# Optimization experiments

Measured on AMD Instinct MI355X. Metric: run time of the kernel, lower is better.

## Reference

```python
import jax, jax.numpy as jnp
import numpy as np

B, T, OBS = 16, 4095, 128
HID, NH, FF, NL = 256, 8, 1024, 4
DH = HID // NH
ACT = 32
KEPS = 0.001   # performer kernel_epsilon (generalized attention default)
LNEPS = 1e-6   # flax LayerNorm default eps


def setup_inputs() -> dict:
    key = jax.random.key(0)
    ks = list(jax.random.split(key, 16))
    s = 0.02
    r = lambda k, shape: jax.random.normal(k, shape, jnp.float32) * s
    return {
        "hidden_state": jnp.zeros((B, 1, HID), jnp.float32),
        "ins": jax.random.normal(ks[0], (B, T, OBS), jnp.float32),
        "resets": jax.random.randint(ks[1], (B,), 0, 2).astype(bool),
        "emb_W": r(ks[2], (OBS, HID)), "emb_b": jnp.zeros((HID,), jnp.float32),
        "Wq": r(ks[3], (NL, HID, NH, DH)), "bq": jnp.zeros((NL, NH, DH), jnp.float32),
        "Wk": r(ks[4], (NL, HID, NH, DH)), "bk": jnp.zeros((NL, NH, DH), jnp.float32),
        "Wv": r(ks[5], (NL, HID, NH, DH)), "bv": jnp.zeros((NL, NH, DH), jnp.float32),
        "Wo": r(ks[6], (NL, NH, DH, HID)), "bo": jnp.zeros((NL, HID), jnp.float32),
        "ln1_s": jnp.ones((NL, HID), jnp.float32), "ln1_b": jnp.zeros((NL, HID), jnp.float32),
        "W1": r(ks[7], (NL, HID, FF)), "b1": jnp.zeros((NL, FF), jnp.float32),
        "W2": r(ks[8], (NL, FF, HID)), "b2": jnp.zeros((NL, HID), jnp.float32),
        "ln2_s": jnp.ones((NL, HID), jnp.float32), "ln2_b": jnp.zeros((NL, HID), jnp.float32),
        "qp_W": r(ks[9], (HID, ACT)), "qp_b": jnp.zeros((ACT,), jnp.float32),
    }


def layer_norm(x, scale, bias):
    m = x.mean(-1, keepdims=True)
    v = ((x - m) ** 2).mean(-1, keepdims=True)
    return (x - m) * jax.lax.rsqrt(v + LNEPS) * scale + bias


def favor_attention(q, k, v):
    # FAVOR+ generalized attention with deterministic relu features (no random
    # projection, make_fast_generalized_attention defaults), bidirectional,
    # renormalized. q,k,v: [B, L, H, Dh]; feature dim M == Dh.
    qp = jax.nn.relu(q) + KEPS
    kp = jax.nn.relu(k) + KEPS
    kv = jnp.einsum('blhm,blhd->bhmd', kp, v)            # [B,H,M,Dh]
    num = jnp.einsum('blhm,bhmd->blhd', qp, kv)           # [B,L,H,Dh]
    den = jnp.einsum('blhm,bhm->blh', qp, kp.sum(axis=1))  # [B,L,H]
    return num / den[..., None]


def encoder_block(x, Wq, bq, Wk, bk, Wv, bv, Wo, bo, ln1_s, ln1_b, W1, b1, W2, b2, ln2_s, ln2_b):
    q = jnp.einsum('bld,dhm->blhm', x, Wq) + bq
    k = jnp.einsum('bld,dhm->blhm', x, Wk) + bk
    v = jnp.einsum('bld,dhm->blhm', x, Wv) + bv
    a = favor_attention(q, k, v)
    o = jnp.einsum('blhm,hmd->bld', a, Wo) + bo
    x = o + o  # faithful to source: x = attn(x); x = x + dropout(x)
    x = layer_norm(x, ln1_s, ln1_b)
    h = jax.nn.relu(x @ W1 + b1) @ W2 + b2
    h = h + h  # same residual quirk on the FFN branch
    return layer_norm(h, ln2_s, ln2_b)


def reference(hidden_state, ins, resets, emb_W, emb_b, Wq, bq, Wk, bk, Wv, bv, Wo, bo, ln1_s, ln1_b, W1, b1, W2, b2, ln2_s, ln2_b, qp_W, qp_b):
    emb = ins @ emb_W + emb_b                         # [B, T, HID]
    hs = jnp.where(resets[:, None, None], 0.0, hidden_state)
    x = jnp.concatenate([hs, emb], axis=-2)           # [B, 1+T, HID]
    for i in range(NL):
        x = encoder_block(x, Wq[i], bq[i], Wk[i], bk[i], Wv[i], bv[i], Wo[i], bo[i],
                          ln1_s[i], ln1_b[i], W1[i], b1[i], W2[i], b2[i], ln2_s[i], ln2_b[i])
    new_hidden = x[..., 0:1, :]                       # carry token
    q_vals = new_hidden @ qp_W + qp_b                 # [B, 1, ACT]
    return new_hidden, q_vals
```

## Files before the change

kernel.cpp:

```cpp
#include <hip/hip_runtime.h>


typedef unsigned short bf16_t;
typedef __attribute__((ext_vector_type(8))) short short8;
typedef __attribute__((ext_vector_type(4))) float float4v;

#define NB 16
#define LSEQ 4096
#define MROWS (NB * LSEQ)
#define HIDD 256
#define NHEAD 8
#define DHEAD 32
#define FFD 1024
#define NLAY 4
#define KEPS_F 1e-3f
#define LNEPS_F 1e-6f
#define KV_ELEMS (NB * NHEAD * 32 * 33)

__device__ __forceinline__ float b2f(bf16_t h) {
    return __uint_as_float(((unsigned int)h) << 16);
}
__device__ __forceinline__ bf16_t f2b(float f) {
    unsigned int u = __float_as_uint(f);
    u += 0x7fffu + ((u >> 16) & 1u);
    return (bf16_t)(u >> 16);
}

#define GLOAD_LDS16(g, l)                                                     \
    __builtin_amdgcn_global_load_lds(                                         \
        (const __attribute__((address_space(1))) void*)(g),                   \
        (__attribute__((address_space(3))) void*)(l), 16, 0, 0)

__global__ __launch_bounds__(256) void conv_transpose_kernel(
    const float* __restrict__ in, bf16_t* __restrict__ out, int R, int C,
    size_t ils, size_t ols)
{
    __shared__ float tile[32][33];
    const size_t ib = (size_t)blockIdx.z * ils;
    const size_t ob = (size_t)blockIdx.z * ols;
    const int r0 = blockIdx.y * 32, c0 = blockIdx.x * 32;
    const int tx = threadIdx.x & 31, ty = threadIdx.x >> 5;
#pragma unroll
    for (int rr = ty; rr < 32; rr += 8)
        tile[rr][tx] = in[ib + (size_t)(r0 + rr) * C + c0 + tx];
    __syncthreads();
#pragma unroll
    for (int rr = ty; rr < 32; rr += 8)
        out[ob + (size_t)(c0 + rr) * R + r0 + tx] = f2b(tile[tx][rr]);
}

__global__ __launch_bounds__(256) void concat_bias_kernel(
    const float* __restrict__ bq, const float* __restrict__ bk,
    const float* __restrict__ bv, float* __restrict__ bqkv)
{
    const int l = blockIdx.x, j = threadIdx.x;
    bqkv[l * 768 + j]       = bq[l * 256 + j];
    bqkv[l * 768 + 256 + j] = bk[l * 256 + j];
    bqkv[l * 768 + 512 + j] = bv[l * 256 + j];
}

__global__ __launch_bounds__(256) void prep_a_kernel(
    const float* __restrict__ ins, bf16_t* __restrict__ Ain)
{
    const int row = blockIdx.x * 2 + (threadIdx.x >> 7);
    const int j = threadIdx.x & 127;
    const int b = row >> 12, l = row & (LSEQ - 1);
    bf16_t v = 0;
    if (l != 0) v = f2b(ins[((size_t)b * 4095 + (l - 1)) * 128 + j]);
    Ain[(size_t)row * 128 + j] = v;
}

__global__ __launch_bounds__(256) void fix_row0_kernel(
    const float* __restrict__ hidden, const int* __restrict__ resets,
    bf16_t* __restrict__ X)
{
    const int b = blockIdx.x, j = threadIdx.x;
    float v = resets[b] ? 0.f : hidden[b * HIDD + j];
    X[((size_t)b * LSEQ) * HIDD + j] = f2b(v);
}

template <int MODE>
__global__ __launch_bounds__(512) void gemm_mfma(
    const bf16_t* __restrict__ A, const bf16_t* __restrict__ WT,
    const float* __restrict__ bias, bf16_t* __restrict__ C,
    int M, int N, int K, int lda, int ldc)
{
    __shared__ __align__(16) bf16_t As[128 * 64];
    __shared__ __align__(16) bf16_t Bs[256 * 64];
    const int tid = threadIdx.x;
    const int wave = tid >> 6, lane = tid & 63;
    const int bm = blockIdx.y * 128, bn = blockIdx.x * 256;
    const int quad = lane >> 4, mr = lane & 15;
    const int mxor = mr & 7;
    const int wm0 = (wave & 1) * 64;
    const int wn0 = (wave >> 1) * 64;

    float4v acc[4][4];
#pragma unroll
    for (int i = 0; i < 4; i++)
#pragma unroll
        for (int j = 0; j < 4; j++) acc[i][j] = (float4v)(0.f);

    for (int k0 = 0; k0 < K; k0 += 64) {
#pragma unroll
        for (int it = 0; it < 2; it++) {
            const int c = it * 512 + tid;
            const int r = c >> 3;
            const int kofs = ((c & 7) ^ (r & 7)) * 8;
            GLOAD_LDS16(A + (size_t)(bm + r) * lda + k0 + kofs, &As[c * 8]);
        }
#pragma unroll
        for (int it = 0; it < 4; it++) {
            const int c = it * 512 + tid;
            const int r = c >> 3;
            const int kofs = ((c & 7) ^ (r & 7)) * 8;
            GLOAD_LDS16(WT + (size_t)(bn + r) * K + k0 + kofs, &Bs[c * 8]);
        }
        __syncthreads();
#pragma unroll
        for (int kk = 0; kk < 8; kk += 4) {
            short8 a[4], b[4];
#pragma unroll
            for (int i = 0; i < 4; i++)
                a[i] = *(const short8*)&As[((wm0 + i * 16 + mr) * 8 + ((quad + kk) ^ mxor)) * 8];
#pragma unroll
            for (int j = 0; j < 4; j++)
                b[j] = *(const short8*)&Bs[((wn0 + j * 16 + mr) * 8 + ((quad + kk) ^ mxor)) * 8];
#pragma unroll
            for (int i = 0; i < 4; i++)
#pragma unroll
                for (int j = 0; j < 4; j++)
                    acc[i][j] = __builtin_amdgcn_mfma_f32_16x16x32_bf16(
                        a[i], b[j], acc[i][j], 0, 0, 0);
        }
        __syncthreads();
    }

    float bcol[4];
#pragma unroll
    for (int j = 0; j < 4; j++) bcol[j] = bias[bn + wn0 + j * 16 + mr];
#pragma unroll
    for (int i = 0; i < 4; i++) {
#pragma unroll
        for (int r = 0; r < 4; r++) {
            const int grow = bm + wm0 + i * 16 + quad * 4 + r;
            bf16_t* crow = C + (size_t)grow * ldc + bn + wn0 + mr;
#pragma unroll
            for (int j = 0; j < 4; j++) {
                float v = acc[i][j][r] + bcol[j];
                if (MODE == 1) v = fmaxf(v, 0.f);
                crow[j * 16] = f2b(v);
            }
        }
    }
}

__global__ __launch_bounds__(512) void gemm_ln_mfma(
    const bf16_t* __restrict__ A, const bf16_t* __restrict__ WT,
    const float* __restrict__ bias, const float* __restrict__ sc,
    const float* __restrict__ bi, bf16_t* __restrict__ out,
    int K, int lda)
{
    __shared__ __align__(16) bf16_t As[128 * 64];
    __shared__ __align__(16) bf16_t Bs[256 * 64];
    __shared__ float red[8][64][2];
    __shared__ float fin[128][2];

    const int tid = threadIdx.x;
    const int wave = tid >> 6, lane = tid & 63;
    const int bm = blockIdx.x * 128;
    const int quad = lane >> 4, mr = lane & 15;
    const int mxor = mr & 7;
    const int wm0 = (wave & 1) * 64;
    const int wn0 = (wave >> 1) * 64;

    float4v acc[4][4];
#pragma unroll
    for (int i = 0; i < 4; i++)
#pragma unroll
        for (int j = 0; j < 4; j++) acc[i][j] = (float4v)(0.f);

    for (int k0 = 0; k0 < K; k0 += 64) {
#pragma unroll
        for (int it = 0; it < 6; it++) {
            const int c = it * 512 + tid;
            if (c < 1024) {
                const int r = c >> 3;
                const int kofs = ((c & 7) ^ (r & 7)) * 8;
                GLOAD_LDS16(A + (size_t)(bm + r) * lda + k0 + kofs, &As[c * 8]);
            } else {
                const int cb = c - 1024;
                const int r = cb >> 3;
                const int kofs = ((cb & 7) ^ (r & 7)) * 8;
                GLOAD_LDS16(WT + (size_t)r * K + k0 + kofs, &Bs[cb * 8]);
            }
        }
        __syncthreads();
#pragma unroll
        for (int kk = 0; kk < 8; kk += 4) {
            short8 a[4], b[4];
#pragma unroll
            for (int i = 0; i < 4; i++)
                a[i] = *(const short8*)&As[((wm0 + i * 16 + mr) * 8 + ((quad + kk) ^ mxor)) * 8];
#pragma unroll
            for (int j = 0; j < 4; j++)
                b[j] = *(const short8*)&Bs[((wn0 + j * 16 + mr) * 8 + ((quad + kk) ^ mxor)) * 8];
#pragma unroll
            for (int i = 0; i < 4; i++)
#pragma unroll
                for (int j = 0; j < 4; j++)
                    acc[i][j] = __builtin_amdgcn_mfma_f32_16x16x32_bf16(
                        a[i], b[j], acc[i][j], 0, 0, 0);
        }
        __syncthreads();
    }

    float bcol[4];
#pragma unroll
    for (int j = 0; j < 4; j++) bcol[j] = bias[wn0 + j * 16 + mr];

#pragma unroll
    for (int i = 0; i < 4; i++) {
#pragma unroll
        for (int r = 0; r < 4; r++) {
            float s = 0.f, s2 = 0.f;
#pragma unroll
            for (int j = 0; j < 4; j++) {
                const float v = 2.0f * (acc[i][j][r] + bcol[j]);
                s += v; s2 += v * v;
            }
#pragma unroll
            for (int off = 1; off < 16; off <<= 1) {
                s  += __shfl_xor(s, off, 64);
                s2 += __shfl_xor(s2, off, 64);
            }
            if (mr == 0) {
                const int rl = i * 16 + quad * 4 + r;
                red[wave][rl][0] = s;
                red[wave][rl][1] = s2;
            }
        }
    }
    __syncthreads();
    if (tid < 256) {
        const int R = tid >> 1, p = tid & 1;
        const int mh = R >> 6, rl = R & 63;
        fin[R][p] = red[mh][rl][p] + red[mh + 2][rl][p]
                  + red[mh + 4][rl][p] + red[mh + 6][rl][p];
    }
    __syncthreads();

    float scv[4], biv[4];
#pragma unroll
    for (int j = 0; j < 4; j++) {
        scv[j] = sc[wn0 + j * 16 + mr];
        biv[j] = bi[wn0 + j * 16 + mr];
    }
#pragma unroll
    for (int i = 0; i < 4; i++) {
#pragma unroll
        for (int r = 0; r < 4; r++) {
            const int R = wm0 + i * 16 + quad * 4 + r;
            const float mean = fin[R][0] * (1.0f / 256.0f);
            const float var  = fin[R][1] * (1.0f / 256.0f) - mean * mean;
            const float rs = rsqrtf(var + LNEPS_F);
            bf16_t* crow = out + (size_t)(bm + R) * 256 + wn0 + mr;
#pragma unroll
            for (int j = 0; j < 4; j++) {
                const float v = 2.0f * (acc[i][j][r] + bcol[j]);
                crow[j * 16] = f2b((v - mean) * rs * scv[j] + biv[j]);
            }
        }
    }
}

__global__ __launch_bounds__(256) void zero_kv(float* __restrict__ KV)
{
    int i = blockIdx.x * 256 + threadIdx.x;
    if (i < KV_ELEMS) KV[i] = 0.f;
}

__global__ __launch_bounds__(256) void kv_mfma(
    const bf16_t* __restrict__ QKV, float* __restrict__ KV)
{
    __shared__ __align__(16) char smem[24576];
    bf16_t (*kp)[36] = (bf16_t(*)[36])smem;
    bf16_t (*vv)[52] = (bf16_t(*)[52])(smem + 9216);
    float (*red)[6][64][4] = (float(*)[6][64][4])smem;

    const int bh = blockIdx.x;
    const int b = bh >> 3, h = bh & 7;
    const size_t rowbase = (size_t)b * LSEQ + blockIdx.y * 512;
    const int tid = threadIdx.x;
    const int wave = tid >> 6, lane = tid & 63;
    const int quad = lane >> 4, mr = lane & 15;

    for (int e = tid; e < 128 * 20; e += 256) {
        const int l = e / 20, c = 32 + (e % 20);
        vv[l][c] = (c == 32) ? (bf16_t)0x3F80 : (bf16_t)0;
    }

    float4v acc[2][3];
#pragma unroll
    for (int i = 0; i < 2; i++)
#pragma unroll
        for (int t = 0; t < 3; t++) acc[i][t] = (float4v)(0.f);

    for (int pass = 0; pass < 4; pass++) {
        __syncthreads();
        const size_t lp = rowbase + pass * 128;
#pragma unroll
        for (int it = 0; it < 4; it++) {
            const int e = tid + it * 256;
            const int l = e >> 3, c0 = (e & 7) * 4;
            const bf16_t* src = QKV + (lp + l) * 768 + 256 + h * 32 + c0;
            ushort4 kq = *(const ushort4*)src;
            ushort4 vq = *(const ushort4*)(src + 256);
            ushort4 ko;
            ko.x = f2b(fmaxf(b2f(kq.x), 0.f) + KEPS_F);
            ko.y = f2b(fmaxf(b2f(kq.y), 0.f) + KEPS_F);
            ko.z = f2b(fmaxf(b2f(kq.z), 0.f) + KEPS_F);
            ko.w = f2b(fmaxf(b2f(kq.w), 0.f) + KEPS_F);
            *(ushort4*)&kp[l][c0] = ko;
            *(ushort4*)&vv[l][c0] = vq;
        }
        __syncthreads();

        const int lw = wave * 32 + quad * 8;
        short8 a[2], bb[3];
#pragma unroll
        for (int i = 0; i < 2; i++)
#pragma unroll
            for (int j = 0; j < 8; j++)
                a[i][j] = (short)kp[lw + j][i * 16 + mr];
#pragma unroll
        for (int t = 0; t < 3; t++)
#pragma unroll
            for (int j = 0; j < 8; j++)
                bb[t][j] = (short)vv[lw + j][t * 16 + mr];
#pragma unroll
        for (int i = 0; i < 2; i++)
#pragma unroll
            for (int t = 0; t < 3; t++)
                acc[i][t] = __builtin_amdgcn_mfma_f32_16x16x32_bf16(
                    a[i], bb[t], acc[i][t], 0, 0, 0);
    }

    __syncthreads();
#pragma unroll
    for (int i = 0; i < 2; i++)
#pragma unroll
        for (int t = 0; t < 3; t++)
#pragma unroll
            for (int r = 0; r < 4; r++)
                red[wave][i * 3 + t][lane][r] = acc[i][t][r];
    __syncthreads();

    float* dst = KV + (size_t)bh * (32 * 33);
    for (int e = tid; e < 6 * 64 * 4; e += 256) {
        const int t = e >> 8, li = (e >> 2) & 63, r = e & 3;
        const float s = red[0][t][li][r] + red[1][t][li][r]
                      + red[2][t][li][r] + red[3][t][li][r];
        const int i = t / 3, j = t % 3;
        const int m = i * 16 + (li >> 4) * 4 + r;
        const int d = j * 16 + (li & 15);
        if (d < 33) atomicAdd(&dst[m * 33 + d], s);
    }
}

#define KVT_MS 40
__global__ __launch_bounds__(256) void favor_mfma(
    bf16_t* __restrict__ QKV, const float* __restrict__ KV)
{
    __shared__ __align__(16) bf16_t kvT[NHEAD * 48 * KVT_MS];
    const int blk = blockIdx.x;
    const int b = blk >> 5;
    const int row0 = b * LSEQ + (blk & 31) * 128;
    const int tid = threadIdx.x;

    for (int e = tid; e < NHEAD * 48 * 32; e += 256) {
        const int h = e / (48 * 32);
        const int rem = e - h * (48 * 32);
        const int d = rem >> 5, m = rem & 31;
        bf16_t v = 0;
        if (d < 33) v = f2b(KV[((size_t)(b * NHEAD + h)) * (32 * 33) + m * 33 + d]);
        kvT[(h * 48 + d) * KVT_MS + m] = v;
    }
    __syncthreads();

    const int wave = tid >> 6, lane = tid & 63;
    const int quad = lane >> 4, mr = lane & 15;
    const int wrow0 = row0 + wave * 32;

    for (int h = 0; h < NHEAD; h++) {
        short8 bf[3];
#pragma unroll
        for (int t = 0; t < 3; t++)
            bf[t] = *(const short8*)&kvT[(h * 48 + t * 16 + mr) * KVT_MS + quad * 8];
#pragma unroll
        for (int mt = 0; mt < 2; mt++) {
            const int r0 = wrow0 + mt * 16;
            short8 araw = *(const short8*)(QKV + (size_t)(r0 + mr) * 768 + h * 32 + quad * 8);
            short8 a;
#pragma unroll
            for (int j = 0; j < 8; j++)
                a[j] = (short)f2b(fmaxf(b2f((bf16_t)araw[j]), 0.f) + KEPS_F);
            float4v c0 = __builtin_amdgcn_mfma_f32_16x16x32_bf16(a, bf[0], (float4v)(0.f), 0, 0, 0);
            float4v c1 = __builtin_amdgcn_mfma_f32_16x16x32_bf16(a, bf[1], (float4v)(0.f), 0, 0, 0);
            float4v c2 = __builtin_amdgcn_mfma_f32_16x16x32_bf16(a, bf[2], (float4v)(0.f), 0, 0, 0);
#pragma unroll
            for (int r = 0; r < 4; r++) {
                const float den = __shfl(c2[r], quad << 4);
                const float rinv = 1.0f / den;
                bf16_t* qrow = QKV + (size_t)(r0 + quad * 4 + r) * 768 + h * 32;
                qrow[mr]      = f2b(c0[r] * rinv);
                qrow[16 + mr] = f2b(c1[r] * rinv);
            }
        }
    }
}

__global__ __launch_bounds__(256) void head_kernel(
    const bf16_t* __restrict__ X, const float* __restrict__ qpW,
    const float* __restrict__ qpb, float* __restrict__ out)
{
    const int b = blockIdx.x, j = threadIdx.x;
    __shared__ float xr[HIDD];
    float v = b2f(X[((size_t)b * LSEQ) * HIDD + j]);
    xr[j] = v;
    out[b * HIDD + j] = v;
    __syncthreads();
    if (j < 32) {
        float acc = qpb[j];
        for (int d = 0; d < HIDD; d++)
            acc = fmaf(xr[d], qpW[d * 32 + j], acc);
        out[NB * HIDD + b * 32 + j] = acc;
    }
}

extern "C" void kernel_launch(void* const* d_in, const int* in_sizes, int n_in,
                              void* d_out, int out_size, void* d_ws, size_t ws_size,
                              hipStream_t stream)
{
    const float* hidden = (const float*)d_in[0];
    const float* ins    = (const float*)d_in[1];
    const int*   resets = (const int*)d_in[2];
    const float* embW   = (const float*)d_in[3];
    const float* embb   = (const float*)d_in[4];
    const float* Wq = (const float*)d_in[5];
    const float* bq = (const float*)d_in[6];
    const float* Wk = (const float*)d_in[7];
    const float* bk = (const float*)d_in[8];
    const float* Wv = (const float*)d_in[9];
    const float* bv = (const float*)d_in[10];
    const float* Wo = (const float*)d_in[11];
    const float* bo = (const float*)d_in[12];
    const float* ln1s = (const float*)d_in[13];
    const float* ln1b = (const float*)d_in[14];
    const float* W1 = (const float*)d_in[15];
    const float* b1 = (const float*)d_in[16];
    const float* W2 = (const float*)d_in[17];
    const float* b2 = (const float*)d_in[18];
    const float* ln2s = (const float*)d_in[19];
    const float* ln2b = (const float*)d_in[20];
    const float* qpW = (const float*)d_in[21];
    const float* qpb = (const float*)d_in[22];

    const size_t ACT_SZ = (size_t)MROWS * HIDD;
    bf16_t* X    = (bf16_t*)d_ws;
    bf16_t* QKV  = X + ACT_SZ;
    bf16_t* H1   = QKV;
    bf16_t* Ain  = QKV;
    float*  KV   = (float*)(QKV + (size_t)MROWS * FFD);
    float*  bqkv = KV + KV_ELEMS;
    bf16_t* WqkvT = (bf16_t*)(bqkv + NLAY * 768);
    bf16_t* WoT   = WqkvT + (size_t)NLAY * 3 * HIDD * HIDD;
    bf16_t* W1T   = WoT + (size_t)NLAY * HIDD * HIDD;
    bf16_t* W2T   = W1T + (size_t)NLAY * HIDD * FFD;
    bf16_t* embWT = W2T + (size_t)NLAY * FFD * HIDD;

    const dim3 blk(256);
    const dim3 blk512(512);
    const size_t HH = (size_t)HIDD * HIDD;

    conv_transpose_kernel<<<dim3(8, 8, NLAY), blk, 0, stream>>>(Wq, WqkvT,          HIDD, HIDD, HH, 3 * HH);
    conv_transpose_kernel<<<dim3(8, 8, NLAY), blk, 0, stream>>>(Wk, WqkvT + HH,     HIDD, HIDD, HH, 3 * HH);
    conv_transpose_kernel<<<dim3(8, 8, NLAY), blk, 0, stream>>>(Wv, WqkvT + 2 * HH, HIDD, HIDD, HH, 3 * HH);
    conv_transpose_kernel<<<dim3(8, 8, NLAY), blk, 0, stream>>>(Wo, WoT, HIDD, HIDD, HH, HH);
    conv_transpose_kernel<<<dim3(32, 8, NLAY), blk, 0, stream>>>(W1, W1T, HIDD, FFD, (size_t)HIDD * FFD, (size_t)HIDD * FFD);
    conv_transpose_kernel<<<dim3(8, 32, NLAY), blk, 0, stream>>>(W2, W2T, FFD, HIDD, (size_t)HIDD * FFD, (size_t)HIDD * FFD);
    conv_transpose_kernel<<<dim3(8, 4, 1), blk, 0, stream>>>(embW, embWT, 128, HIDD, 0, 0);
    concat_bias_kernel<<<NLAY, blk, 0, stream>>>(bq, bk, bv, bqkv);

    prep_a_kernel<<<MROWS / 2, blk, 0, stream>>>(ins, Ain);
    gemm_mfma<0><<<dim3(1, 512), blk512, 0, stream>>>(Ain, embWT, embb, X, MROWS, HIDD, 128, 128, HIDD);
    fix_row0_kernel<<<NB, blk, 0, stream>>>(hidden, resets, X);

    for (int l = 0; l < NLAY; l++) {
        gemm_mfma<0><<<dim3(3, 512), blk512, 0, stream>>>(X, WqkvT + (size_t)l * 3 * HH,
                                                          bqkv + l * 768, QKV, MROWS, 768, HIDD, HIDD, 768);

        zero_kv<<<(KV_ELEMS + 255) / 256, blk, 0, stream>>>(KV);
        kv_mfma<<<dim3(NB * NHEAD, 8), blk, 0, stream>>>(QKV, KV);
        favor_mfma<<<NB * 32, blk, 0, stream>>>(QKV, KV);

        gemm_ln_mfma<<<MROWS / 128, blk512, 0, stream>>>(
            QKV, WoT + (size_t)l * HH, bo + l * HIDD,
            ln1s + l * HIDD, ln1b + l * HIDD, X, HIDD, 768);

        gemm_mfma<1><<<dim3(4, 512), blk512, 0, stream>>>(X, W1T + (size_t)l * HIDD * FFD,
                                                          b1 + l * FFD, H1, MROWS, FFD, HIDD, HIDD, FFD);
        gemm_ln_mfma<<<MROWS / 128, blk512, 0, stream>>>(
            H1, W2T + (size_t)l * FFD * HIDD, b2 + l * HIDD,
            ln2s + l * HIDD, ln2b + l * HIDD, X, FFD, FFD);
    }

    head_kernel<<<NB, blk, 0, stream>>>(X, qpW, qpb, (float*)d_out);
}
```

Measured before the change: 1.045 ms.

## Fuse FAVOR attention normalization into output-projection GEMM with LayerNorm

Removes the separate favor_mfma kernel and computes the relu-feature query times KV and the denominator division inside the Wo GEMM prologue, writing the normalized attention straight into the shared-memory A tile. This avoids writing the attention output back to QKV in global memory and reading it again in the projection GEMM. Each GEMM block now reloads the per-batch KV matrix into LDS and does extra MFMA work per k-step. The larger LDS footprint may lower occupancy.

```diff
diff --git a/kernel.cpp b/kernel.cpp
--- a/kernel.cpp
+++ b/kernel.cpp
@@ -211,6 +211,161 @@
                 for (int j = 0; j < 4; j++)
                     acc[i][j] = __builtin_amdgcn_mfma_f32_16x16x32_bf16(
                         a[i], b[j], acc[i][j], 0, 0, 0);
+        }
+        __syncthreads();
+    }
+
+    float bcol[4];
+#pragma unroll
+    for (int j = 0; j < 4; j++) bcol[j] = bias[wn0 + j * 16 + mr];
+
+#pragma unroll
+    for (int i = 0; i < 4; i++) {
+#pragma unroll
+        for (int r = 0; r < 4; r++) {
+            float s = 0.f, s2 = 0.f;
+#pragma unroll
+            for (int j = 0; j < 4; j++) {
+                const float v = 2.0f * (acc[i][j][r] + bcol[j]);
+                s += v; s2 += v * v;
+            }
+#pragma unroll
+            for (int off = 1; off < 16; off <<= 1) {
+                s  += __shfl_xor(s, off, 64);
+                s2 += __shfl_xor(s2, off, 64);
+            }
+            if (mr == 0) {
+                const int rl = i * 16 + quad * 4 + r;
+                red[wave][rl][0] = s;
+                red[wave][rl][1] = s2;
+            }
+        }
+    }
+    __syncthreads();
+    if (tid < 256) {
+        const int R = tid >> 1, p = tid & 1;
+        const int mh = R >> 6, rl = R & 63;
+        fin[R][p] = red[mh][rl][p] + red[mh + 2][rl][p]
+                  + red[mh + 4][rl][p] + red[mh + 6][rl][p];
+    }
+    __syncthreads();
+
+    float scv[4], biv[4];
+#pragma unroll
+    for (int j = 0; j < 4; j++) {
+        scv[j] = sc[wn0 + j * 16 + mr];
+        biv[j] = bi[wn0 + j * 16 + mr];
+    }
+#pragma unroll
+    for (int i = 0; i < 4; i++) {
+#pragma unroll
+        for (int r = 0; r < 4; r++) {
+            const int R = wm0 + i * 16 + quad * 4 + r;
+            const float mean = fin[R][0] * (1.0f / 256.0f);
+            const float var  = fin[R][1] * (1.0f / 256.0f) - mean * mean;
+            const float rs = rsqrtf(var + LNEPS_F);
+            bf16_t* crow = out + (size_t)(bm + R) * 256 + wn0 + mr;
+#pragma unroll
+            for (int j = 0; j < 4; j++) {
+                const float v = 2.0f * (acc[i][j][r] + bcol[j]);
+                crow[j * 16] = f2b((v - mean) * rs * scv[j] + biv[j]);
+            }
+        }
+    }
+}
+
+__global__ __launch_bounds__(512) void gemm_favor_ln_mfma(
+    const bf16_t* __restrict__ QKV, const float* __restrict__ KV,
+    const bf16_t* __restrict__ WT, const float* __restrict__ bias,
+    const float* __restrict__ sc, const float* __restrict__ bi,
+    bf16_t* __restrict__ out)
+{
+    __shared__ __align__(16) bf16_t As[128 * 64];
+    __shared__ __align__(16) bf16_t Bs[256 * 64];
+    __shared__ __align__(16) bf16_t kvT[NHEAD * 34 * 36];
+    __shared__ float red[8][64][2];
+    __shared__ float fin[128][2];
+
+    const int tid = threadIdx.x;
+    const int wave = tid >> 6, lane = tid & 63;
+    const int bm = blockIdx.x * 128;
+    const int b = bm >> 12;
+    const int quad = lane >> 4, mr = lane & 15;
+    const int mxor = mr & 7;
+    const int wm0 = (wave & 1) * 64;
+    const int wn0 = (wave >> 1) * 64;
+
+    for (int e = tid; e < NHEAD * 34 * 32; e += 512) {
+        const int h = e / (34 * 32);
+        const int rem = e - h * (34 * 32);
+        const int d = rem >> 5, m = rem & 31;
+        bf16_t v = 0;
+        if (d < 33) v = f2b(KV[((size_t)(b * NHEAD + h)) * (32 * 33) + m * 33 + d]);
+        kvT[(h * 34 + d) * 36 + m] = v;
+    }
+    __syncthreads();
+
+    float4v acc[4][4];
+#pragma unroll
+    for (int i = 0; i < 4; i++)
+#pragma unroll
+        for (int j = 0; j < 4; j++) acc[i][j] = (float4v)(0.f);
+
+    for (int k0 = 0; k0 < 256; k0 += 64) {
+#pragma unroll
+        for (int it = 0; it < 4; it++) {
+            const int c = it * 512 + tid;
+            const int r = c >> 3;
+            const int kofs = ((c & 7) ^ (r & 7)) * 8;
+            GLOAD_LDS16(WT + (size_t)r * 256 + k0 + kofs, &Bs[c * 8]);
+        }
+        const int h0 = k0 >> 5;
+        const int Rrow = bm + wave * 16 + mr;
+#pragma unroll
+        for (int hh = 0; hh < 2; hh++) {
+            const int h = h0 + hh;
+            short8 araw = *(const short8*)(QKV + (size_t)Rrow * 768 + h * 32 + quad * 8);
+            short8 a;
+#pragma unroll
+            for (int j = 0; j < 8; j++)
+                a[j] = (short)f2b(fmaxf(b2f((bf16_t)araw[j]), 0.f) + KEPS_F);
+            short8 bf0 = *(const short8*)&kvT[(h * 34 + mr) * 36 + quad * 8];
+            short8 bf1 = *(const short8*)&kvT[(h * 34 + 16 + mr) * 36 + quad * 8];
+            short8 bden;
+#pragma unroll
+            for (int j = 0; j < 8; j++) bden[j] = 0;
+            if (mr == 0)
+                bden = *(const short8*)&kvT[(h * 34 + 32) * 36 + quad * 8];
+            float4v c0 = __builtin_amdgcn_mfma_f32_16x16x32_bf16(a, bf0, (float4v)(0.f), 0, 0, 0);
+            float4v c1 = __builtin_amdgcn_mfma_f32_16x16x32_bf16(a, bf1, (float4v)(0.f), 0, 0, 0);
+            float4v c2 = __builtin_amdgcn_mfma_f32_16x16x32_bf16(a, bden, (float4v)(0.f), 0, 0, 0);
+#pragma unroll
+            for (int r = 0; r < 4; r++) {
+                const float den = __shfl(c2[r], quad << 4);
+                const float rinv = 1.0f / den;
+                const int R = wave * 16 + quad * 4 + r;
+                const int ca = hh * 32 + mr;
+                const int cbn = hh * 32 + 16 + mr;
+                As[(R * 8 + ((ca >> 3) ^ (R & 7))) * 8 + (ca & 7)]   = f2b(c0[r] * rinv);
+                As[(R * 8 + ((cbn >> 3) ^ (R & 7))) * 8 + (cbn & 7)] = f2b(c1[r] * rinv);
+            }
+        }
+        __syncthreads();
+#pragma unroll
+        for (int kk = 0; kk < 8; kk += 4) {
+            short8 a[4], bfr[4];
+#pragma unroll
+            for (int i = 0; i < 4; i++)
+                a[i] = *(const short8*)&As[((wm0 + i * 16 + mr) * 8 + ((quad + kk) ^ mxor)) * 8];
+#pragma unroll
+            for (int j = 0; j < 4; j++)
+                bfr[j] = *(const short8*)&Bs[((wn0 + j * 16 + mr) * 8 + ((quad + kk) ^ mxor)) * 8];
+#pragma unroll
+            for (int i = 0; i < 4; i++)
+#pragma unroll
+                for (int j = 0; j < 4; j++)
+                    acc[i][j] = __builtin_amdgcn_mfma_f32_16x16x32_bf16(
+                        a[i], bfr[j], acc[i][j], 0, 0, 0);
         }
         __syncthreads();
     }
@@ -365,58 +520,6 @@
         const int m = i * 16 + (li >> 4) * 4 + r;
         const int d = j * 16 + (li & 15);
         if (d < 33) atomicAdd(&dst[m * 33 + d], s);
-    }
-}
-
-#define KVT_MS 40
-__global__ __launch_bounds__(256) void favor_mfma(
-    bf16_t* __restrict__ QKV, const float* __restrict__ KV)
-{
-    __shared__ __align__(16) bf16_t kvT[NHEAD * 48 * KVT_MS];
-    const int blk = blockIdx.x;
-    const int b = blk >> 5;
-    const int row0 = b * LSEQ + (blk & 31) * 128;
-    const int tid = threadIdx.x;
-
-    for (int e = tid; e < NHEAD * 48 * 32; e += 256) {
-        const int h = e / (48 * 32);
-        const int rem = e - h * (48 * 32);
-        const int d = rem >> 5, m = rem & 31;
-        bf16_t v = 0;
-        if (d < 33) v = f2b(KV[((size_t)(b * NHEAD + h)) * (32 * 33) + m * 33 + d]);
-        kvT[(h * 48 + d) * KVT_MS + m] = v;
-    }
-    __syncthreads();
-
-    const int wave = tid >> 6, lane = tid & 63;
-    const int quad = lane >> 4, mr = lane & 15;
-    const int wrow0 = row0 + wave * 32;
-
-    for (int h = 0; h < NHEAD; h++) {
-        short8 bf[3];
-#pragma unroll
-        for (int t = 0; t < 3; t++)
-            bf[t] = *(const short8*)&kvT[(h * 48 + t * 16 + mr) * KVT_MS + quad * 8];
-#pragma unroll
-        for (int mt = 0; mt < 2; mt++) {
-            const int r0 = wrow0 + mt * 16;
-            short8 araw = *(const short8*)(QKV + (size_t)(r0 + mr) * 768 + h * 32 + quad * 8);
-            short8 a;
-#pragma unroll
-            for (int j = 0; j < 8; j++)
-                a[j] = (short)f2b(fmaxf(b2f((bf16_t)araw[j]), 0.f) + KEPS_F);
-            float4v c0 = __builtin_amdgcn_mfma_f32_16x16x32_bf16(a, bf[0], (float4v)(0.f), 0, 0, 0);
-            float4v c1 = __builtin_amdgcn_mfma_f32_16x16x32_bf16(a, bf[1], (float4v)(0.f), 0, 0, 0);
-            float4v c2 = __builtin_amdgcn_mfma_f32_16x16x32_bf16(a, bf[2], (float4v)(0.f), 0, 0, 0);
-#pragma unroll
-            for (int r = 0; r < 4; r++) {
-                const float den = __shfl(c2[r], quad << 4);
-                const float rinv = 1.0f / den;
-                bf16_t* qrow = QKV + (size_t)(r0 + quad * 4 + r) * 768 + h * 32;
-                qrow[mr]      = f2b(c0[r] * rinv);
-                qrow[16 + mr] = f2b(c1[r] * rinv);
-            }
-        }
     }
 }
 
@@ -502,11 +605,10 @@
 
         zero_kv<<<(KV_ELEMS + 255) / 256, blk, 0, stream>>>(KV);
         kv_mfma<<<dim3(NB * NHEAD, 8), blk, 0, stream>>>(QKV, KV);
-        favor_mfma<<<NB * 32, blk, 0, stream>>>(QKV, KV);
-
-        gemm_ln_mfma<<<MROWS / 128, blk512, 0, stream>>>(
-            QKV, WoT + (size_t)l * HH, bo + l * HIDD,
-            ln1s + l * HIDD, ln1b + l * HIDD, X, HIDD, 768);
+
+        gemm_favor_ln_mfma<<<MROWS / 128, blk512, 0, stream>>>(
+            QKV, KV, WoT + (size_t)l * HH, bo + l * HIDD,
+            ln1s + l * HIDD, ln1b + l * HIDD, X);
 
         gemm_mfma<1><<<dim3(4, 512), blk512, 0, stream>>>(X, W1T + (size_t)l * HIDD * FFD,
                                                           b1 + l * FFD, H1, MROWS, FFD, HIDD, HIDD, FFD);
```

Result: faster. 1.024 ms (-2.0%).
